# Optimization experiments

Measured on AMD Instinct MI355X. Metric: run time of the kernel, lower is better.

## Reference

```python
import jax, jax.numpy as jnp
import numpy as np

N = 4096
IN_DIM = 6
HID = 32
HEADS1 = 4
OUT_DIM = 64


def _gat_layer(x, mask, W, a_src, a_dst, b):
    # x: [n, in], W: [in, heads*d], a_src/a_dst: [heads, d], b: [heads*d]
    n = x.shape[0]
    heads, d = a_src.shape
    h = (x @ W).reshape(n, heads, d)                      # [n, heads, d]
    e_src = jnp.einsum('nhd,hd->nh', h, a_src)            # [n, heads]
    e_dst = jnp.einsum('nhd,hd->nh', h, a_dst)            # [n, heads]
    logits = e_src[:, None, :] + e_dst[None, :, :]        # [n, n, heads]
    logits = jax.nn.leaky_relu(logits, negative_slope=0.2)
    logits = jnp.where(mask[:, :, None], logits, jnp.float32(-1e9))
    alpha = jax.nn.softmax(logits, axis=1)                # softmax over j (dim=1)
    # dropout disabled (eval mode reference)
    out = jnp.einsum('ijh,jhd->ihd', alpha, h).reshape(n, heads * d)
    return out + b


def setup_inputs() -> dict:
    key = jax.random.key(0)
    ks = jax.random.split(key, 10)
    x = jax.random.normal(ks[0], (N, IN_DIM), dtype=jnp.float32)
    adj = jax.random.bernoulli(ks[1], 0.01, (N, N)).astype(jnp.float32)
    s = 0.1
    W1 = jax.random.normal(ks[2], (IN_DIM, HEADS1 * HID), dtype=jnp.float32) * s
    a_src1 = jax.random.normal(ks[3], (HEADS1, HID), dtype=jnp.float32) * s
    a_dst1 = jax.random.normal(ks[4], (HEADS1, HID), dtype=jnp.float32) * s
    b1 = jnp.zeros((HEADS1 * HID,), dtype=jnp.float32)
    W2 = jax.random.normal(ks[5], (HEADS1 * HID, OUT_DIM), dtype=jnp.float32) * s
    a_src2 = jax.random.normal(ks[6], (1, OUT_DIM), dtype=jnp.float32) * s
    a_dst2 = jax.random.normal(ks[7], (1, OUT_DIM), dtype=jnp.float32) * s
    b2 = jnp.zeros((OUT_DIM,), dtype=jnp.float32)
    return {'x': x, 'adj': adj, 'W1': W1, 'a_src1': a_src1, 'a_dst1': a_dst1,
            'b1': b1, 'W2': W2, 'a_src2': a_src2, 'a_dst2': a_dst2, 'b2': b2}


def reference(x, adj, W1, a_src1, a_dst1, b1, W2, a_src2, a_dst2, b2):
    n = x.shape[0]
    # add self loops: a = max(a, I), mask = a > 0
    a = jnp.maximum(adj, jnp.eye(n, dtype=adj.dtype))
    mask = a > 0
    h1 = jax.nn.elu(_gat_layer(x, mask, W1, a_src1, a_dst1, b1))
    # dropout disabled (eval mode)
    h2 = _gat_layer(h1, mask, W2, a_src2, a_dst2, b2)
    return h2
```

## Files before the change

### kernel.cpp

```cpp
#include <hip/hip_runtime.h>
#include <hip/hip_bf16.h>

#define N 4096
#define IN_DIM 6
#define HID 32
#define HEADS1 4
#define D1 (HEADS1*HID)
#define OUT_DIM 64
#define MAXNB 192

__global__ void k1_h1pre(const float* __restrict__ x,
                         const float* __restrict__ W1,
                         const float* __restrict__ a_src1,
                         const float* __restrict__ a_dst1,
                         float* __restrict__ hpre,
                         float* __restrict__ es1,
                         float* __restrict__ ed1) {
    int i = blockIdx.x;
    int t = threadIdx.x;
    __shared__ float xs[IN_DIM];
    if (t < IN_DIM) xs[t] = x[i*IN_DIM + t];
    __syncthreads();
    float acc = 0.f;
    #pragma unroll
    for (int k = 0; k < IN_DIM; ++k)
        acc += xs[k] * W1[k*D1 + t];
    hpre[(size_t)i*D1 + t] = acc;
    float ps = acc * a_src1[t];
    float pd = acc * a_dst1[t];
    #pragma unroll
    for (int off = 16; off >= 1; off >>= 1) {
        ps += __shfl_xor(ps, off, 64);
        pd += __shfl_xor(pd, off, 64);
    }
    if ((t & 31) == 0) {
        int h = t >> 5;
        es1[i*HEADS1 + h] = ps;
        ed1[i*HEADS1 + h] = pd;
    }
}

__global__ void k2_csr(const float* __restrict__ adj,
                       int* __restrict__ cnt, int* __restrict__ idxg) {
    int i = blockIdx.x;
    int t = threadIdx.x;
    __shared__ int c;
    __shared__ int list[MAXNB];
    if (t == 0) c = 0;
    __syncthreads();
    const float4* row = (const float4*)(adj + (size_t)i * N);
    for (int k = t; k < N/4; k += 256) {
        float4 v = row[k];
        float f[4] = {v.x, v.y, v.z, v.w};
        #pragma unroll
        for (int q = 0; q < 4; ++q) {
            int j = k*4 + q;
            if (f[q] > 0.f || j == i) {
                int p = atomicAdd(&c, 1);
                if (p < MAXNB) list[p] = j;
            }
        }
    }
    __syncthreads();
    int cc = min(c, MAXNB);
    if (t == 0) cnt[i] = cc;
    for (int p = t; p < cc; p += 256) idxg[i*MAXNB + p] = list[p];
}

__global__ void k3_agg1(const float* __restrict__ hpre,
                        const float* __restrict__ es1,
                        const float* __restrict__ ed1,
                        const int* __restrict__ cnt,
                        const int* __restrict__ idxg,
                        const float* __restrict__ b1,
                        float* __restrict__ h1) {
    int i = blockIdx.x;
    int t = threadIdx.x;
    int c = cnt[i];
    __shared__ int js[MAXNB];
    __shared__ float alpha[HEADS1][MAXNB];
    __shared__ float esi[HEADS1];
    if (t < HEADS1) esi[t] = es1[i*HEADS1 + t];
    for (int p = t; p < c; p += 128) js[p] = idxg[i*MAXNB + p];
    __syncthreads();
    for (int p = t; p < c; p += 128) {
        int j = js[p];
        #pragma unroll
        for (int h = 0; h < HEADS1; ++h) {
            float l = esi[h] + ed1[j*HEADS1 + h];
            alpha[h][p] = (l > 0.f) ? l : 0.2f*l;
        }
    }
    __syncthreads();
    int h = t >> 5, lane = t & 31;
    float m = -1e30f;
    for (int p = lane; p < c; p += 32) m = fmaxf(m, alpha[h][p]);
    #pragma unroll
    for (int off = 16; off >= 1; off >>= 1) m = fmaxf(m, __shfl_xor(m, off, 64));
    float s = 0.f;
    for (int p = lane; p < c; p += 32) s += __expf(alpha[h][p] - m);
    #pragma unroll
    for (int off = 16; off >= 1; off >>= 1) s += __shfl_xor(s, off, 64);
    float inv = 1.f / s;
    for (int p = lane; p < c; p += 32) alpha[h][p] = __expf(alpha[h][p] - m) * inv;
    __syncthreads();
    float acc = 0.f;
    for (int p = 0; p < c; ++p)
        acc += alpha[h][p] * hpre[(size_t)js[p]*D1 + t];
    acc += b1[t];
    h1[(size_t)i*D1 + t] = (acc > 0.f) ? acc : expm1f(acc);
}

__global__ void k4_h2pre(const float* __restrict__ h1,
                         const float* __restrict__ W2,
                         const float* __restrict__ a_src2,
                         const float* __restrict__ a_dst2,
                         float* __restrict__ h2pre,
                         float* __restrict__ es2,
                         float* __restrict__ ed2) {
    int i = blockIdx.x;
    int t = threadIdx.x;
    __shared__ float hs[D1];
    hs[t]      = h1[(size_t)i*D1 + t];
    hs[t + 64] = h1[(size_t)i*D1 + t + 64];
    __syncthreads();
    float acc = 0.f;
    #pragma unroll
    for (int k = 0; k < D1; ++k)
        acc += hs[k] * W2[k*OUT_DIM + t];
    h2pre[(size_t)i*OUT_DIM + t] = acc;
    float ps = acc * a_src2[t];
    float pd = acc * a_dst2[t];
    #pragma unroll
    for (int off = 32; off >= 1; off >>= 1) {
        ps += __shfl_xor(ps, off, 64);
        pd += __shfl_xor(pd, off, 64);
    }
    if (t == 0) { es2[i] = ps; ed2[i] = pd; }
}

__global__ void k5_agg2(const float* __restrict__ h2pre,
                        const float* __restrict__ es2,
                        const float* __restrict__ ed2,
                        const int* __restrict__ cnt,
                        const int* __restrict__ idxg,
                        const float* __restrict__ b2v,
                        float* __restrict__ out) {
    int i = blockIdx.x;
    int t = threadIdx.x;
    int c = cnt[i];
    __shared__ int js[MAXNB];
    __shared__ float alpha[MAXNB];
    for (int p = t; p < c; p += 64) js[p] = idxg[i*MAXNB + p];
    __syncthreads();
    float esi = es2[i];
    float m = -1e30f;
    for (int p = t; p < c; p += 64) {
        float l = esi + ed2[js[p]];
        l = (l > 0.f) ? l : 0.2f*l;
        alpha[p] = l;
        m = fmaxf(m, l);
    }
    #pragma unroll
    for (int off = 32; off >= 1; off >>= 1) m = fmaxf(m, __shfl_xor(m, off, 64));
    __syncthreads();
    float s = 0.f;
    for (int p = t; p < c; p += 64) s += __expf(alpha[p] - m);
    #pragma unroll
    for (int off = 32; off >= 1; off >>= 1) s += __shfl_xor(s, off, 64);
    float inv = 1.f / s;
    for (int p = t; p < c; p += 64) alpha[p] = __expf(alpha[p] - m) * inv;
    __syncthreads();
    float acc = 0.f;
    for (int p = 0; p < c; ++p)
        acc += alpha[p] * h2pre[(size_t)js[p]*OUT_DIM + t];
    acc += b2v[t];
    out[(size_t)i*OUT_DIM + t] = acc;
}

extern "C" void kernel_launch(void* const* d_in, const int* in_sizes, int n_in,
                              void* d_out, int out_size, void* d_ws, size_t ws_size,
                              hipStream_t stream) {
    const float* x      = (const float*)d_in[0];
    const float* adj    = (const float*)d_in[1];
    const float* W1     = (const float*)d_in[2];
    const float* a_src1 = (const float*)d_in[3];
    const float* a_dst1 = (const float*)d_in[4];
    const float* b1     = (const float*)d_in[5];
    const float* W2     = (const float*)d_in[6];
    const float* a_src2 = (const float*)d_in[7];
    const float* a_dst2 = (const float*)d_in[8];
    const float* b2v    = (const float*)d_in[9];
    float* out = (float*)d_out;

    float* ws    = (float*)d_ws;
    float* hpre  = ws;
    float* h1    = hpre  + (size_t)N*D1;
    float* h2pre = h1    + (size_t)N*D1;
    float* es1   = h2pre + (size_t)N*OUT_DIM;
    float* ed1   = es1   + (size_t)N*HEADS1;
    float* es2   = ed1   + (size_t)N*HEADS1;
    float* ed2   = es2   + N;
    int*   cnt   = (int*)(ed2 + N);
    int*   idxg  = cnt + N;

    k1_h1pre<<<N, 128, 0, stream>>>(x, W1, a_src1, a_dst1, hpre, es1, ed1);
    k2_csr  <<<N, 256, 0, stream>>>(adj, cnt, idxg);
    k3_agg1 <<<N, 128, 0, stream>>>(hpre, es1, ed1, cnt, idxg, b1, h1);
    k4_h2pre<<<N,  64, 0, stream>>>(h1, W2, a_src2, a_dst2, h2pre, es2, ed2);
    k5_agg2 <<<N,  64, 0, stream>>>(h2pre, es2, ed2, cnt, idxg, b2v, out);
}
```

Measured before the change: 135.9 us.

## Fuse five GAT kernels into three and split gather accumulators

Merges the layer-1 projection into the adjacency-scan kernel, and the layer-2 projection into the layer-1 aggregation kernel, so h1 stays in shared memory instead of round-tripping through global memory. This cuts the launch count from five to three. The gather loops now use two independent accumulators to expose more memory-level parallelism. In exchange, the fused kernels need extra shared memory and barriers, and the W2 projection is split across two half-blocks whose partial sums are combined in shared memory.

```diff
diff --git a/kernel.cpp b/kernel.cpp
--- a/kernel.cpp
+++ b/kernel.cpp
@@ -9,45 +9,26 @@
 #define OUT_DIM 64
 #define MAXNB 192
 
-__global__ void k1_h1pre(const float* __restrict__ x,
-                         const float* __restrict__ W1,
-                         const float* __restrict__ a_src1,
-                         const float* __restrict__ a_dst1,
-                         float* __restrict__ hpre,
-                         float* __restrict__ es1,
-                         float* __restrict__ ed1) {
+__global__ __launch_bounds__(256) void kA(
+        const float* __restrict__ x,
+        const float* __restrict__ W1,
+        const float* __restrict__ a_src1,
+        const float* __restrict__ a_dst1,
+        const float* __restrict__ adj,
+        float* __restrict__ hpre,
+        float* __restrict__ es1,
+        float* __restrict__ ed1,
+        int* __restrict__ cnt,
+        int* __restrict__ idxg) {
     int i = blockIdx.x;
     int t = threadIdx.x;
     __shared__ float xs[IN_DIM];
-    if (t < IN_DIM) xs[t] = x[i*IN_DIM + t];
-    __syncthreads();
-    float acc = 0.f;
-    #pragma unroll
-    for (int k = 0; k < IN_DIM; ++k)
-        acc += xs[k] * W1[k*D1 + t];
-    hpre[(size_t)i*D1 + t] = acc;
-    float ps = acc * a_src1[t];
-    float pd = acc * a_dst1[t];
-    #pragma unroll
-    for (int off = 16; off >= 1; off >>= 1) {
-        ps += __shfl_xor(ps, off, 64);
-        pd += __shfl_xor(pd, off, 64);
-    }
-    if ((t & 31) == 0) {
-        int h = t >> 5;
-        es1[i*HEADS1 + h] = ps;
-        ed1[i*HEADS1 + h] = pd;
-    }
-}
-
-__global__ void k2_csr(const float* __restrict__ adj,
-                       int* __restrict__ cnt, int* __restrict__ idxg) {
-    int i = blockIdx.x;
-    int t = threadIdx.x;
     __shared__ int c;
     __shared__ int list[MAXNB];
     if (t == 0) c = 0;
-    __syncthreads();
+    if (t < IN_DIM) xs[t] = x[i*IN_DIM + t];
+    __syncthreads();
+
     const float4* row = (const float4*)(adj + (size_t)i * N);
     for (int k = t; k < N/4; k += 256) {
         float4 v = row[k];
@@ -61,25 +42,53 @@
             }
         }
     }
+
+    if (t < 128) {
+        float acc = 0.f;
+        #pragma unroll
+        for (int k = 0; k < IN_DIM; ++k)
+            acc += xs[k] * W1[k*D1 + t];
+        hpre[(size_t)i*D1 + t] = acc;
+        float ps = acc * a_src1[t];
+        float pd = acc * a_dst1[t];
+        #pragma unroll
+        for (int off = 16; off >= 1; off >>= 1) {
+            ps += __shfl_xor(ps, off, 64);
+            pd += __shfl_xor(pd, off, 64);
+        }
+        if ((t & 31) == 0) {
+            int h = t >> 5;
+            es1[i*HEADS1 + h] = ps;
+            ed1[i*HEADS1 + h] = pd;
+        }
+    }
     __syncthreads();
     int cc = min(c, MAXNB);
     if (t == 0) cnt[i] = cc;
     for (int p = t; p < cc; p += 256) idxg[i*MAXNB + p] = list[p];
 }
 
-__global__ void k3_agg1(const float* __restrict__ hpre,
-                        const float* __restrict__ es1,
-                        const float* __restrict__ ed1,
-                        const int* __restrict__ cnt,
-                        const int* __restrict__ idxg,
-                        const float* __restrict__ b1,
-                        float* __restrict__ h1) {
+__global__ __launch_bounds__(128) void kB(
+        const float* __restrict__ hpre,
+        const float* __restrict__ es1,
+        const float* __restrict__ ed1,
+        const int* __restrict__ cnt,
+        const int* __restrict__ idxg,
+        const float* __restrict__ b1,
+        const float* __restrict__ W2,
+        const float* __restrict__ a_src2,
+        const float* __restrict__ a_dst2,
+        float* __restrict__ h2pre,
+        float* __restrict__ es2,
+        float* __restrict__ ed2) {
     int i = blockIdx.x;
     int t = threadIdx.x;
     int c = cnt[i];
     __shared__ int js[MAXNB];
     __shared__ float alpha[HEADS1][MAXNB];
     __shared__ float esi[HEADS1];
+    __shared__ float h1s[D1];
+    __shared__ float psum[2][OUT_DIM];
     if (t < HEADS1) esi[t] = es1[i*HEADS1 + t];
     for (int p = t; p < c; p += 128) js[p] = idxg[i*MAXNB + p];
     __syncthreads();
@@ -104,48 +113,45 @@
     float inv = 1.f / s;
     for (int p = lane; p < c; p += 32) alpha[h][p] = __expf(alpha[h][p] - m) * inv;
     __syncthreads();
-    float acc = 0.f;
-    for (int p = 0; p < c; ++p)
-        acc += alpha[h][p] * hpre[(size_t)js[p]*D1 + t];
-    acc += b1[t];
-    h1[(size_t)i*D1 + t] = (acc > 0.f) ? acc : expm1f(acc);
-}
-
-__global__ void k4_h2pre(const float* __restrict__ h1,
-                         const float* __restrict__ W2,
-                         const float* __restrict__ a_src2,
-                         const float* __restrict__ a_dst2,
-                         float* __restrict__ h2pre,
-                         float* __restrict__ es2,
-                         float* __restrict__ ed2) {
-    int i = blockIdx.x;
-    int t = threadIdx.x;
-    __shared__ float hs[D1];
-    hs[t]      = h1[(size_t)i*D1 + t];
-    hs[t + 64] = h1[(size_t)i*D1 + t + 64];
-    __syncthreads();
-    float acc = 0.f;
-    #pragma unroll
-    for (int k = 0; k < D1; ++k)
-        acc += hs[k] * W2[k*OUT_DIM + t];
-    h2pre[(size_t)i*OUT_DIM + t] = acc;
-    float ps = acc * a_src2[t];
-    float pd = acc * a_dst2[t];
-    #pragma unroll
-    for (int off = 32; off >= 1; off >>= 1) {
-        ps += __shfl_xor(ps, off, 64);
-        pd += __shfl_xor(pd, off, 64);
-    }
-    if (t == 0) { es2[i] = ps; ed2[i] = pd; }
-}
-
-__global__ void k5_agg2(const float* __restrict__ h2pre,
-                        const float* __restrict__ es2,
-                        const float* __restrict__ ed2,
-                        const int* __restrict__ cnt,
-                        const int* __restrict__ idxg,
-                        const float* __restrict__ b2v,
-                        float* __restrict__ out) {
+    float acc0 = 0.f, acc1 = 0.f;
+    int p = 0;
+    for (; p + 2 <= c; p += 2) {
+        acc0 += alpha[h][p]   * hpre[(size_t)js[p]  *D1 + t];
+        acc1 += alpha[h][p+1] * hpre[(size_t)js[p+1]*D1 + t];
+    }
+    if (p < c) acc0 += alpha[h][p] * hpre[(size_t)js[p]*D1 + t];
+    float acc = acc0 + acc1 + b1[t];
+    h1s[t] = (acc > 0.f) ? acc : expm1f(acc);
+    __syncthreads();
+    int o = t & 63, half = t >> 6;
+    float a2 = 0.f;
+    #pragma unroll
+    for (int k = 0; k < 64; ++k)
+        a2 += h1s[half*64 + k] * W2[(half*64 + k)*OUT_DIM + o];
+    psum[half][o] = a2;
+    __syncthreads();
+    if (t < 64) {
+        float val = psum[0][t] + psum[1][t];
+        h2pre[(size_t)i*OUT_DIM + t] = val;
+        float ps = val * a_src2[t];
+        float pd = val * a_dst2[t];
+        #pragma unroll
+        for (int off = 32; off >= 1; off >>= 1) {
+            ps += __shfl_xor(ps, off, 64);
+            pd += __shfl_xor(pd, off, 64);
+        }
+        if (t == 0) { es2[i] = ps; ed2[i] = pd; }
+    }
+}
+
+__global__ __launch_bounds__(64) void kC(
+        const float* __restrict__ h2pre,
+        const float* __restrict__ es2,
+        const float* __restrict__ ed2,
+        const int* __restrict__ cnt,
+        const int* __restrict__ idxg,
+        const float* __restrict__ b2v,
+        float* __restrict__ out) {
     int i = blockIdx.x;
     int t = threadIdx.x;
     int c = cnt[i];
@@ -171,11 +177,14 @@
     float inv = 1.f / s;
     for (int p = t; p < c; p += 64) alpha[p] = __expf(alpha[p] - m) * inv;
     __syncthreads();
-    float acc = 0.f;
-    for (int p = 0; p < c; ++p)
-        acc += alpha[p] * h2pre[(size_t)js[p]*OUT_DIM + t];
-    acc += b2v[t];
-    out[(size_t)i*OUT_DIM + t] = acc;
+    float acc0 = 0.f, acc1 = 0.f;
+    int p = 0;
+    for (; p + 2 <= c; p += 2) {
+        acc0 += alpha[p]   * h2pre[(size_t)js[p]  *OUT_DIM + t];
+        acc1 += alpha[p+1] * h2pre[(size_t)js[p+1]*OUT_DIM + t];
+    }
+    if (p < c) acc0 += alpha[p] * h2pre[(size_t)js[p]*OUT_DIM + t];
+    out[(size_t)i*OUT_DIM + t] = acc0 + acc1 + b2v[t];
 }
 
 extern "C" void kernel_launch(void* const* d_in, const int* in_sizes, int n_in,
@@ -195,8 +204,7 @@
 
     float* ws    = (float*)d_ws;
     float* hpre  = ws;
-    float* h1    = hpre  + (size_t)N*D1;
-    float* h2pre = h1    + (size_t)N*D1;
+    float* h2pre = hpre  + (size_t)N*D1;
     float* es1   = h2pre + (size_t)N*OUT_DIM;
     float* ed1   = es1   + (size_t)N*HEADS1;
     float* es2   = ed1   + (size_t)N*HEADS1;
@@ -204,9 +212,8 @@
     int*   cnt   = (int*)(ed2 + N);
     int*   idxg  = cnt + N;
 
-    k1_h1pre<<<N, 128, 0, stream>>>(x, W1, a_src1, a_dst1, hpre, es1, ed1);
-    k2_csr  <<<N, 256, 0, stream>>>(adj, cnt, idxg);
-    k3_agg1 <<<N, 128, 0, stream>>>(hpre, es1, ed1, cnt, idxg, b1, h1);
-    k4_h2pre<<<N,  64, 0, stream>>>(h1, W2, a_src2, a_dst2, h2pre, es2, ed2);
-    k5_agg2 <<<N,  64, 0, stream>>>(h2pre, es2, ed2, cnt, idxg, b2v, out);
-}
+    kA<<<N, 256, 0, stream>>>(x, W1, a_src1, a_dst1, adj, hpre, es1, ed1, cnt, idxg);
+    kB<<<N, 128, 0, stream>>>(hpre, es1, ed1, cnt, idxg, b1, W2, a_src2, a_dst2,
+                              h2pre, es2, ed2);
+    kC<<<N,  64, 0, stream>>>(h2pre, es2, ed2, cnt, idxg, b2v, out);
+}
```

New measurement: 138.4 us. About the same (+1.8%).
